# Kernel optimization log

Hardware: AMD Instinct MI355X
Metric: run time of the kernel (lower is better)

Reference implementation:

```python
import jax, jax.numpy as jnp
import numpy as np

ALPHA = 100.0  # superspike surrogate sharpness (fwd uses hard heaviside)
DT = 0.001
TAU_SYN_INV = 200.0
TAU_MEM_INV = 100.0
V_LEAK = 0.0
V_TH = 1.0
V_RESET = 0.0

@jax.custom_vjp
def heaviside(x):
    return (x > 0).astype(x.dtype)

def _heaviside_fwd(x):
    return heaviside(x), x

def _heaviside_bwd(x, g):
    # norse 'super' (SuperSpike) surrogate gradient
    return (g / (ALPHA * jnp.abs(x) + 1.0) ** 2,)

heaviside.defvjp(_heaviside_fwd, _heaviside_bwd)


def setup_inputs() -> dict:
    key = jax.random.key(0)
    k1, k2 = jax.random.split(key)
    T, B, F = 1024, 128, 512
    input_spikes = jax.random.uniform(k1, (T, B, F), dtype=jnp.float32)
    bound = 1.0 / np.sqrt(F)
    W = jax.random.uniform(k2, (F, F), minval=-bound, maxval=bound, dtype=jnp.float32)
    return {"input_spikes": input_spikes, "W": W}


def reference(input_spikes, W):
    # fc applied per timestep is equivalent to one batched contraction over time
    xs = jnp.einsum('tbf,gf->tbg', input_spikes, W)  # [T,B,F]
    B, F = input_spikes.shape[1], input_spikes.shape[2]

    def step(carry, x_t):
        v, i = carry
        v_decayed = v + DT * TAU_MEM_INV * ((V_LEAK - v) + i)
        i_decayed = i + (-DT * TAU_SYN_INV) * i
        z = heaviside(v_decayed - V_TH)
        v_new = (1.0 - z) * v_decayed + z * V_RESET
        i_new = i_decayed + x_t
        return (v_new, i_new), z

    init = (jnp.zeros((B, F), input_spikes.dtype), jnp.zeros((B, F), input_spikes.dtype))
    (v_final, i_final), zs = jax.lax.scan(step, init, xs)
    z_final = zs[-1]
    # original returns (z, LIFState(z, v, i))
    return z_final, z_final, v_final, i_final
```

## Files before the change

kernel.cpp:

```cpp
#include <hip/hip_runtime.h>


#define T_DIM 1024
#define B_DIM 128
#define F_DIM 512
#define NB (B_DIM * F_DIM)

#define TM 128
#define TN 256
#define KC 16
#define LDA_S 132
#define LDB_S 260
#define A_SZ (KC * LDA_S)
#define B_SZ (KC * LDB_S)

__global__ __launch_bounds__(256, 2)
void gemm_kernel(const float* __restrict__ A, const float* __restrict__ W,
                 float* __restrict__ C) {
    __shared__ float As[2 * A_SZ];
    __shared__ float Bs[2 * B_SZ];
    const int tid = threadIdx.x;
    const int m0 = blockIdx.x * TM;
    const int n0 = blockIdx.y * TN;
    const int tn4 = (tid & 15) * 4;
    const int tm4 = (tid >> 4) * 4;
    const int srow = tid >> 2;
    const int sk = (tid & 3) * 4;

    float acc[8][16];
    #pragma unroll
    for (int i = 0; i < 8; ++i)
        #pragma unroll
        for (int j = 0; j < 16; ++j) acc[i][j] = 0.f;

    {
        float4 av[2], bv[4];
        #pragma unroll
        for (int p = 0; p < 2; ++p)
            av[p] = *(const float4*)(A + (size_t)(m0 + srow + 64 * p) * F_DIM + sk);
        #pragma unroll
        for (int p = 0; p < 4; ++p)
            bv[p] = *(const float4*)(W + (size_t)(n0 + srow + 64 * p) * F_DIM + sk);
        #pragma unroll
        for (int p = 0; p < 2; ++p) {
            const int r = srow + 64 * p;
            As[(sk + 0) * LDA_S + r] = av[p].x;  As[(sk + 1) * LDA_S + r] = av[p].y;
            As[(sk + 2) * LDA_S + r] = av[p].z;  As[(sk + 3) * LDA_S + r] = av[p].w;
        }
        #pragma unroll
        for (int p = 0; p < 4; ++p) {
            const int r = srow + 64 * p;
            Bs[(sk + 0) * LDB_S + r] = bv[p].x;  Bs[(sk + 1) * LDB_S + r] = bv[p].y;
            Bs[(sk + 2) * LDB_S + r] = bv[p].z;  Bs[(sk + 3) * LDB_S + r] = bv[p].w;
        }
        __syncthreads();
    }

    int cur = 0;
    for (int k0 = 0; k0 < F_DIM; k0 += KC) {
        const bool more = (k0 + KC < F_DIM);
        float4 av[2], bv[4];
        if (more) {
            #pragma unroll
            for (int p = 0; p < 2; ++p)
                av[p] = *(const float4*)(A + (size_t)(m0 + srow + 64 * p) * F_DIM
                                           + (k0 + KC) + sk);
            #pragma unroll
            for (int p = 0; p < 4; ++p)
                bv[p] = *(const float4*)(W + (size_t)(n0 + srow + 64 * p) * F_DIM
                                           + (k0 + KC) + sk);
        }

        const float* asb = As + cur * A_SZ;
        const float* bsb = Bs + cur * B_SZ;
        #pragma unroll 4
        for (int k = 0; k < KC; ++k) {
            const float4 a0 = *(const float4*)(asb + k * LDA_S + tm4);
            const float4 a1 = *(const float4*)(asb + k * LDA_S + tm4 + 64);
            const float4 b0 = *(const float4*)(bsb + k * LDB_S + tn4);
            const float4 b1 = *(const float4*)(bsb + k * LDB_S + tn4 + 64);
            const float4 b2 = *(const float4*)(bsb + k * LDB_S + tn4 + 128);
            const float4 b3 = *(const float4*)(bsb + k * LDB_S + tn4 + 192);
            const float a[8] = {a0.x, a0.y, a0.z, a0.w, a1.x, a1.y, a1.z, a1.w};
            const float b[16] = {b0.x, b0.y, b0.z, b0.w, b1.x, b1.y, b1.z, b1.w,
                                 b2.x, b2.y, b2.z, b2.w, b3.x, b3.y, b3.z, b3.w};
            #pragma unroll
            for (int i = 0; i < 8; ++i)
                #pragma unroll
                for (int j = 0; j < 16; ++j)
                    acc[i][j] += a[i] * b[j];
        }

        if (more) {
            float* asn = As + (cur ^ 1) * A_SZ;
            float* bsn = Bs + (cur ^ 1) * B_SZ;
            #pragma unroll
            for (int p = 0; p < 2; ++p) {
                const int r = srow + 64 * p;
                asn[(sk + 0) * LDA_S + r] = av[p].x;  asn[(sk + 1) * LDA_S + r] = av[p].y;
                asn[(sk + 2) * LDA_S + r] = av[p].z;  asn[(sk + 3) * LDA_S + r] = av[p].w;
            }
            #pragma unroll
            for (int p = 0; p < 4; ++p) {
                const int r = srow + 64 * p;
                bsn[(sk + 0) * LDB_S + r] = bv[p].x;  bsn[(sk + 1) * LDB_S + r] = bv[p].y;
                bsn[(sk + 2) * LDB_S + r] = bv[p].z;  bsn[(sk + 3) * LDB_S + r] = bv[p].w;
            }
            __syncthreads();
            cur ^= 1;
        }
    }

    #pragma unroll
    for (int i = 0; i < 8; ++i) {
        const int m = m0 + ((i < 4) ? (tm4 + i) : (tm4 + 60 + i));
        #pragma unroll
        for (int q = 0; q < 4; ++q) {
            const float4 c = make_float4(acc[i][4 * q + 0], acc[i][4 * q + 1],
                                         acc[i][4 * q + 2], acc[i][4 * q + 3]);
            *(float4*)(C + (size_t)m * F_DIM + n0 + tn4 + 64 * q) = c;
        }
    }
}

#define DEPTH 32

__global__ __launch_bounds__(256)
void scan_kernel(const float* __restrict__ xs, float* __restrict__ vi,
                 float* __restrict__ out, int Tc, int first, int last) {
    const int j = blockIdx.x * 256 + threadIdx.x;
    float v, cur;
    if (first) { v = 0.f; cur = 0.f; }
    else       { v = vi[j]; cur = vi[NB + j]; }
    float z = 0.f;
    const float* pj = xs + j;

    if (Tc >= DEPTH && (Tc % DEPTH) == 0) {
        float buf[DEPTH];
        #pragma unroll
        for (int d = 0; d < DEPTH; ++d) buf[d] = pj[(size_t)d * NB];
        for (int tt = 0; tt < Tc; tt += DEPTH) {
            #pragma unroll
            for (int d = 0; d < DEPTH; ++d) {
                const float x = buf[d];
                int tn = tt + DEPTH + d;
                tn = (tn < Tc) ? tn : 0;
                buf[d] = pj[(size_t)tn * NB];
                const float vd = __fadd_rn(v, __fmul_rn(0.1f, __fsub_rn(cur, v)));
                const float id = __fadd_rn(cur, __fmul_rn(-0.2f, cur));
                const bool sp = vd > 1.0f;
                z = sp ? 1.f : 0.f;
                v = sp ? 0.f : vd;
                cur = __fadd_rn(id, x);
            }
        }
    } else {
        for (int t = 0; t < Tc; ++t) {
            const float x = pj[(size_t)t * NB];
            const float vd = __fadd_rn(v, __fmul_rn(0.1f, __fsub_rn(cur, v)));
            const float id = __fadd_rn(cur, __fmul_rn(-0.2f, cur));
            const bool sp = vd > 1.0f;
            z = sp ? 1.f : 0.f;
            v = sp ? 0.f : vd;
            cur = __fadd_rn(id, x);
        }
    }

    if (last) {
        out[j]           = z;
        out[NB + j]      = z;
        out[2 * NB + j]  = v;
        out[3 * NB + j]  = cur;
    } else {
        vi[j]      = v;
        vi[NB + j] = cur;
    }
}

extern "C" void kernel_launch(void* const* d_in, const int* in_sizes, int n_in,
                              void* d_out, int out_size, void* d_ws, size_t ws_size,
                              hipStream_t stream) {
    const float* S = (const float*)d_in[0];
    const float* W = (const float*)d_in[1];
    float* out = (float*)d_out;
    float* vi = (float*)d_ws;
    float* xs = vi + 2 * NB;
    const size_t avail_f = (ws_size / 4 > (size_t)(2 * NB)) ? ws_size / 4 - 2 * NB : 0;
    int Tc = T_DIM;
    while (Tc > 1 && (size_t)Tc * NB > avail_f) Tc >>= 1;
    const int nc = T_DIM / Tc;
    for (int c = 0; c < nc; ++c) {
        const int M = Tc * B_DIM;
        dim3 grid(M / TM, F_DIM / TN);
        gemm_kernel<<<grid, 256, 0, stream>>>(S + (size_t)c * Tc * NB, W, xs);
        scan_kernel<<<NB / 256, 256, 0, stream>>>(xs, vi, out, Tc,
                                                  (c == 0) ? 1 : 0,
                                                  (c == nc - 1) ? 1 : 0);
    }
}
```

Before: 1.031 ms.

## Pre-transpose W and stream B operand from global into registers, skipping LDS

Adds a transpose kernel that writes W^T to workspace. The GEMM then reads B fragments straight from global memory (L2-resident) into registers with a two-slot prefetch, instead of staging them through shared memory. This cuts the LDS stores, the LDS reads and the shared-memory footprint per block, which may allow more occupancy, but it relies on L2/L1 bandwidth for the repeated W reads and adds register pressure. The scan prefetch depth is also raised from 32 to 64.

```diff
diff --git a/kernel.cpp b/kernel.cpp
--- a/kernel.cpp
+++ b/kernel.cpp
@@ -6,19 +6,35 @@
 #define F_DIM 512
 #define NB (B_DIM * F_DIM)
 
+__global__ __launch_bounds__(256)
+void transpose_kernel(const float* __restrict__ W, float* __restrict__ Wt) {
+    __shared__ float t[64][65];
+    const int bx = blockIdx.x, by = blockIdx.y;
+    const int c = threadIdx.x & 63;
+    const int r0 = (threadIdx.x >> 6) * 16;
+    #pragma unroll
+    for (int i = 0; i < 16; ++i) {
+        const int row = r0 + i;
+        t[row][c] = W[(size_t)(by * 64 + row) * F_DIM + bx * 64 + c];
+    }
+    __syncthreads();
+    #pragma unroll
+    for (int i = 0; i < 16; ++i) {
+        const int row = r0 + i;
+        Wt[(size_t)(bx * 64 + row) * F_DIM + by * 64 + c] = t[c][row];
+    }
+}
+
 #define TM 128
 #define TN 256
 #define KC 16
 #define LDA_S 132
-#define LDB_S 260
 #define A_SZ (KC * LDA_S)
-#define B_SZ (KC * LDB_S)
 
 __global__ __launch_bounds__(256, 2)
-void gemm_kernel(const float* __restrict__ A, const float* __restrict__ W,
+void gemm_kernel(const float* __restrict__ A, const float* __restrict__ Wt,
                  float* __restrict__ C) {
     __shared__ float As[2 * A_SZ];
-    __shared__ float Bs[2 * B_SZ];
     const int tid = threadIdx.x;
     const int m0 = blockIdx.x * TM;
     const int n0 = blockIdx.y * TN;
@@ -33,83 +49,82 @@
         #pragma unroll
         for (int j = 0; j < 16; ++j) acc[i][j] = 0.f;
 
+    const float* wp = Wt + n0 + tn4;
+
+    float4 be[4], bo[4];
+    #pragma unroll
+    for (int q = 0; q < 4; ++q)
+        be[q] = *(const float4*)(wp + 64 * q);
+
     {
-        float4 av[2], bv[4];
+        float4 av[2];
         #pragma unroll
         for (int p = 0; p < 2; ++p)
             av[p] = *(const float4*)(A + (size_t)(m0 + srow + 64 * p) * F_DIM + sk);
-        #pragma unroll
-        for (int p = 0; p < 4; ++p)
-            bv[p] = *(const float4*)(W + (size_t)(n0 + srow + 64 * p) * F_DIM + sk);
         #pragma unroll
         for (int p = 0; p < 2; ++p) {
             const int r = srow + 64 * p;
             As[(sk + 0) * LDA_S + r] = av[p].x;  As[(sk + 1) * LDA_S + r] = av[p].y;
             As[(sk + 2) * LDA_S + r] = av[p].z;  As[(sk + 3) * LDA_S + r] = av[p].w;
         }
-        #pragma unroll
-        for (int p = 0; p < 4; ++p) {
-            const int r = srow + 64 * p;
-            Bs[(sk + 0) * LDB_S + r] = bv[p].x;  Bs[(sk + 1) * LDB_S + r] = bv[p].y;
-            Bs[(sk + 2) * LDB_S + r] = bv[p].z;  Bs[(sk + 3) * LDB_S + r] = bv[p].w;
-        }
         __syncthreads();
+    }
+
+#define COMPUTE_K(KK, BSLOT)                                                   \
+    {                                                                          \
+        const float4 a0 = *(const float4*)(asb + (KK) * LDA_S + tm4);          \
+        const float4 a1 = *(const float4*)(asb + (KK) * LDA_S + tm4 + 64);     \
+        const float a[8] = {a0.x, a0.y, a0.z, a0.w, a1.x, a1.y, a1.z, a1.w};   \
+        const float b[16] = {BSLOT[0].x, BSLOT[0].y, BSLOT[0].z, BSLOT[0].w,   \
+                             BSLOT[1].x, BSLOT[1].y, BSLOT[1].z, BSLOT[1].w,   \
+                             BSLOT[2].x, BSLOT[2].y, BSLOT[2].z, BSLOT[2].w,   \
+                             BSLOT[3].x, BSLOT[3].y, BSLOT[3].z, BSLOT[3].w};  \
+        _Pragma("unroll")                                                      \
+        for (int i = 0; i < 8; ++i)                                            \
+            _Pragma("unroll")                                                  \
+            for (int j = 0; j < 16; ++j)                                       \
+                acc[i][j] += a[i] * b[j];                                      \
     }
 
     int cur = 0;
     for (int k0 = 0; k0 < F_DIM; k0 += KC) {
         const bool more = (k0 + KC < F_DIM);
-        float4 av[2], bv[4];
+        float4 av[2];
         if (more) {
             #pragma unroll
             for (int p = 0; p < 2; ++p)
                 av[p] = *(const float4*)(A + (size_t)(m0 + srow + 64 * p) * F_DIM
                                            + (k0 + KC) + sk);
-            #pragma unroll
-            for (int p = 0; p < 4; ++p)
-                bv[p] = *(const float4*)(W + (size_t)(n0 + srow + 64 * p) * F_DIM
-                                           + (k0 + KC) + sk);
         }
 
         const float* asb = As + cur * A_SZ;
-        const float* bsb = Bs + cur * B_SZ;
-        #pragma unroll 4
-        for (int k = 0; k < KC; ++k) {
-            const float4 a0 = *(const float4*)(asb + k * LDA_S + tm4);
-            const float4 a1 = *(const float4*)(asb + k * LDA_S + tm4 + 64);
-            const float4 b0 = *(const float4*)(bsb + k * LDB_S + tn4);
-            const float4 b1 = *(const float4*)(bsb + k * LDB_S + tn4 + 64);
-            const float4 b2 = *(const float4*)(bsb + k * LDB_S + tn4 + 128);
-            const float4 b3 = *(const float4*)(bsb + k * LDB_S + tn4 + 192);
-            const float a[8] = {a0.x, a0.y, a0.z, a0.w, a1.x, a1.y, a1.z, a1.w};
-            const float b[16] = {b0.x, b0.y, b0.z, b0.w, b1.x, b1.y, b1.z, b1.w,
-                                 b2.x, b2.y, b2.z, b2.w, b3.x, b3.y, b3.z, b3.w};
-            #pragma unroll
-            for (int i = 0; i < 8; ++i)
-                #pragma unroll
-                for (int j = 0; j < 16; ++j)
-                    acc[i][j] += a[i] * b[j];
+        #pragma unroll
+        for (int kk = 0; kk < KC; kk += 2) {
+            const int k = k0 + kk;
+            #pragma unroll
+            for (int q = 0; q < 4; ++q)
+                bo[q] = *(const float4*)(wp + (size_t)(k + 1) * F_DIM + 64 * q);
+            COMPUTE_K(kk, be)
+            const int kn = (k + 2 < F_DIM) ? (k + 2) : 0;
+            #pragma unroll
+            for (int q = 0; q < 4; ++q)
+                be[q] = *(const float4*)(wp + (size_t)kn * F_DIM + 64 * q);
+            COMPUTE_K(kk + 1, bo)
         }
 
         if (more) {
             float* asn = As + (cur ^ 1) * A_SZ;
-            float* bsn = Bs + (cur ^ 1) * B_SZ;
             #pragma unroll
             for (int p = 0; p < 2; ++p) {
                 const int r = srow + 64 * p;
                 asn[(sk + 0) * LDA_S + r] = av[p].x;  asn[(sk + 1) * LDA_S + r] = av[p].y;
                 asn[(sk + 2) * LDA_S + r] = av[p].z;  asn[(sk + 3) * LDA_S + r] = av[p].w;
             }
-            #pragma unroll
-            for (int p = 0; p < 4; ++p) {
-                const int r = srow + 64 * p;
-                bsn[(sk + 0) * LDB_S + r] = bv[p].x;  bsn[(sk + 1) * LDB_S + r] = bv[p].y;
-                bsn[(sk + 2) * LDB_S + r] = bv[p].z;  bsn[(sk + 3) * LDB_S + r] = bv[p].w;
-            }
             __syncthreads();
             cur ^= 1;
         }
     }
+#undef COMPUTE_K
 
     #pragma unroll
     for (int i = 0; i < 8; ++i) {
@@ -123,7 +138,7 @@
     }
 }
 
-#define DEPTH 32
+#define DEPTH 64
 
 __global__ __launch_bounds__(256)
 void scan_kernel(const float* __restrict__ xs, float* __restrict__ vi,
@@ -184,15 +199,20 @@
     const float* W = (const float*)d_in[1];
     float* out = (float*)d_out;
     float* vi = (float*)d_ws;
-    float* xs = vi + 2 * NB;
-    const size_t avail_f = (ws_size / 4 > (size_t)(2 * NB)) ? ws_size / 4 - 2 * NB : 0;
+    float* Wt = vi + 2 * NB;
+    float* xs = Wt + (size_t)F_DIM * F_DIM;
+    const size_t used = (size_t)2 * NB + (size_t)F_DIM * F_DIM;
+    const size_t avail_f = (ws_size / 4 > used) ? ws_size / 4 - used : 0;
     int Tc = T_DIM;
     while (Tc > 1 && (size_t)Tc * NB > avail_f) Tc >>= 1;
     const int nc = T_DIM / Tc;
+
+    transpose_kernel<<<dim3(8, 8), 256, 0, stream>>>(W, Wt);
+
     for (int c = 0; c < nc; ++c) {
         const int M = Tc * B_DIM;
         dim3 grid(M / TM, F_DIM / TN);
-        gemm_kernel<<<grid, 256, 0, stream>>>(S + (size_t)c * Tc * NB, W, xs);
+        gemm_kernel<<<grid, 256, 0, stream>>>(S + (size_t)c * Tc * NB, Wt, xs);
         scan_kernel<<<NB / 256, 256, 0, stream>>>(xs, vi, out, Tc,
                                                   (c == 0) ? 1 : 0,
                                                   (c == nc - 1) ? 1 : 0);
```

After: 3.681 ms. 3.57x slower.
